# Optimization experiments

Measured on AMD Instinct MI355X. Metric: run time of the kernel, lower is better.

Reference implementation:

```python
import jax, jax.numpy as jnp
import numpy as np

B = 1024          # batch of subject-object pairs
D_IN_HALF = 2048  # sbj/obj feature width; cat -> input_len = 4096
D_OUT = 1024      # output_len (embedding / label-vec width)
N_LABELS = 128    # number of relation labels in codebook


def setup_inputs() -> dict:
    key = jax.random.key(0)
    ks = jax.random.split(key, 7)
    s = 0.02  # small init scale for weights
    return {
        "sbj_vec": jax.random.normal(ks[0], (B, D_IN_HALF), jnp.float32),
        "obj_vec": jax.random.normal(ks[1], (B, D_IN_HALF), jnp.float32),
        "W1": jax.random.normal(ks[2], (2 * D_IN_HALF, D_OUT), jnp.float32) * s,
        "b1": jax.random.normal(ks[3], (D_OUT,), jnp.float32) * s,
        "W2": jax.random.normal(ks[4], (D_OUT, D_OUT), jnp.float32) * s,
        "b2": jax.random.normal(ks[5], (D_OUT,), jnp.float32) * s,
        "label_vecs": jax.random.normal(ks[6], (N_LABELS, D_OUT), jnp.float32),
    }


def reference(sbj_vec, obj_vec, W1, b1, W2, b2, label_vecs):
    # Sequential(ReLU, Dropout(eval=identity), Linear) applied twice.
    x = jnp.concatenate([sbj_vec, obj_vec], axis=1)          # [B, 2*D_IN_HALF]
    hidden = jax.nn.relu(x) @ W1 + b1                        # [B, D_OUT]
    emb = jax.nn.relu(hidden) @ W2 + b2                      # [B, D_OUT]
    # order_sim vs every label vector, fully batched (replaces per-sample loop):
    # sim[b, l] = -|| relu(label_vecs[l] - emb[b]) ||_2
    diff = jax.nn.relu(label_vecs[None, :, :] - emb[:, None, :])  # [B, L, D_OUT]
    scores = -jnp.sqrt(jnp.sum(diff * diff, axis=2))              # [B, L]
    return scores
```

## Files before the change

### kernel.cpp

```cpp
#include <hip/hip_runtime.h>
#include <math.h>

constexpr int Bn = 1024, DH = 2048, K1 = 4096, DO = 1024, NL = 128;
constexpr int MN = Bn * DO;

typedef __bf16 bf16x8 __attribute__((ext_vector_type(8)));
typedef short  s16x8  __attribute__((ext_vector_type(8)));
typedef float  f32x4  __attribute__((ext_vector_type(4)));

__device__ __forceinline__ unsigned short f2bf(float f) {
  union { float f; unsigned u; } v; v.f = f;
  unsigned r = v.u + 0x7FFFu + ((v.u >> 16) & 1u);
  return (unsigned short)(r >> 16);
}

__global__ __launch_bounds__(256)
void prep(const float* __restrict__ sbj, const float* __restrict__ obj,
          const float* __restrict__ W1, const float* __restrict__ W2,
          unsigned short* __restrict__ Abf,
          unsigned short* __restrict__ W1t, unsigned short* __restrict__ W2t) {
  const int tid = threadIdx.x;
  if (blockIdx.x < 2048) {
    const int t = blockIdx.x * 256 + tid;
    const int m = t >> 9;
    const int k = (t & 511) << 3;
    const float* src = (k < DH) ? sbj + (size_t)m * DH + k
                                : obj + (size_t)m * DH + (k - DH);
    const float4 a = ((const float4*)src)[0];
    const float4 b = ((const float4*)src)[1];
    uint4 o;
    o.x = (unsigned)f2bf(fmaxf(a.x, 0.f)) | ((unsigned)f2bf(fmaxf(a.y, 0.f)) << 16);
    o.y = (unsigned)f2bf(fmaxf(a.z, 0.f)) | ((unsigned)f2bf(fmaxf(a.w, 0.f)) << 16);
    o.z = (unsigned)f2bf(fmaxf(b.x, 0.f)) | ((unsigned)f2bf(fmaxf(b.y, 0.f)) << 16);
    o.w = (unsigned)f2bf(fmaxf(b.z, 0.f)) | ((unsigned)f2bf(fmaxf(b.w, 0.f)) << 16);
    *(uint4*)&Abf[(size_t)m * K1 + k] = o;
    return;
  }
  __shared__ float tl[64][65];
  const int tb = blockIdx.x - 2048;
  int by = tb >> 4;
  const int c0 = (tb & 15) * 64;
  const float* in; unsigned short* out; int R;
  if (by < 64) { in = W1; out = W1t; R = K1; }
  else         { in = W2; out = W2t; R = DO; by -= 64; }
  const int r0 = by * 64;
  {
    const int rr = tid >> 4, cc = (tid & 15) * 4;
    #pragma unroll
    for (int i = 0; i < 4; ++i) {
      const float4 v = *(const float4*)&in[(size_t)(r0 + rr + i * 16) * DO + c0 + cc];
      tl[rr + i * 16][cc + 0] = v.x; tl[rr + i * 16][cc + 1] = v.y;
      tl[rr + i * 16][cc + 2] = v.z; tl[rr + i * 16][cc + 3] = v.w;
    }
  }
  __syncthreads();
  {
    const int r4 = (tid & 15) * 4;
    #pragma unroll
    for (int i = 0; i < 4; ++i) {
      const int cr = i * 16 + (tid >> 4);
      uint2 o;
      o.x = (unsigned)f2bf(tl[r4 + 0][cr]) | ((unsigned)f2bf(tl[r4 + 1][cr]) << 16);
      o.y = (unsigned)f2bf(tl[r4 + 2][cr]) | ((unsigned)f2bf(tl[r4 + 3][cr]) << 16);
      *(uint2*)&out[(size_t)(c0 + cr) * R + r0 + r4] = o;
    }
  }
}

template <int KSLICE>
__global__ __launch_bounds__(256, 4)
void mfma_gemm(const unsigned short* __restrict__ A,
               const unsigned short* __restrict__ Bt,
               float* __restrict__ P, int K) {
  __shared__ __align__(16) unsigned short smem[2 * 64 * 128];
  unsigned short* LA = smem;
  unsigned short* LB = smem + 64 * 128;

  const int tid = threadIdx.x;
  const int w = tid >> 6, l = tid & 63;

  const int bid = blockIdx.x;
  const int g = bid & 7, t = bid >> 3;
  const int x = (g & 3) * 4 + (t & 3);
  const int y = (g >> 2) * 8 + ((t >> 2) & 7);
  const int z = t >> 5;
  const int m0 = y * 64, n0 = x * 64;
  const int kb = z * KSLICE;

  f32x4 acc[4][4] = {};

  constexpr int NIT = KSLICE / 128;
  for (int it = 0; it < NIT; ++it) {
    const int k0 = kb + it * 128;
    #pragma unroll
    for (int i = 0; i < 4; ++i) {
      const int c = i * 256 + tid, m = c >> 4, kc = c & 15;
      const int kcg = (kc & 8) | ((kc & 7) ^ (m & 7));
      __builtin_amdgcn_global_load_lds(
          (const __attribute__((address_space(1))) unsigned int*)(A + (size_t)(m0 + m) * K + k0 + kcg * 8),
          (__attribute__((address_space(3))) unsigned int*)&LA[c * 8], 16, 0, 0);
    }
    #pragma unroll
    for (int i = 0; i < 4; ++i) {
      const int c = i * 256 + tid, n = c >> 4, kc = c & 15;
      const int kcg = (kc & 8) | ((kc & 7) ^ (n & 7));
      __builtin_amdgcn_global_load_lds(
          (const __attribute__((address_space(1))) unsigned int*)(Bt + (size_t)(n0 + n) * K + k0 + kcg * 8),
          (__attribute__((address_space(3))) unsigned int*)&LB[c * 8], 16, 0, 0);
    }
    __syncthreads();

    const int kcq = w * 4 + (l >> 4);
    bf16x8 af[4], bfr[4];
    #pragma unroll
    for (int i = 0; i < 4; ++i) {
      const int r = i * 16 + (l & 15);
      const int kca = (kcq & 8) | ((kcq & 7) ^ (r & 7));
      af[i]  = __builtin_bit_cast(bf16x8, *(const s16x8*)&LA[(r * 16 + kca) * 8]);
      bfr[i] = __builtin_bit_cast(bf16x8, *(const s16x8*)&LB[(r * 16 + kca) * 8]);
    }
    #pragma unroll
    for (int i = 0; i < 4; ++i)
      #pragma unroll
      for (int j = 0; j < 4; ++j)
        acc[i][j] = __builtin_amdgcn_mfma_f32_16x16x32_bf16(af[i], bfr[j], acc[i][j], 0, 0, 0);
    __syncthreads();
  }

  float* red = (float*)smem;
  if (w >= 2) {
    #pragma unroll
    for (int i = 0; i < 4; ++i)
      #pragma unroll
      for (int j = 0; j < 4; ++j)
        *(f32x4*)&red[(w - 2) * 4096 + ((i * 4 + j) * 64 + l) * 4] = acc[i][j];
  }
  __syncthreads();
  if (w < 2) {
    #pragma unroll
    for (int i = 0; i < 4; ++i)
      #pragma unroll
      for (int j = 0; j < 4; ++j)
        acc[i][j] += *(const f32x4*)&red[w * 4096 + ((i * 4 + j) * 64 + l) * 4];
  }
  __syncthreads();
  if (w == 1) {
    #pragma unroll
    for (int i = 0; i < 2; ++i)
      #pragma unroll
      for (int j = 0; j < 4; ++j)
        *(f32x4*)&red[((i * 4 + j) * 64 + l) * 4] = acc[i][j];
  } else if (w == 0) {
    #pragma unroll
    for (int i = 0; i < 2; ++i)
      #pragma unroll
      for (int j = 0; j < 4; ++j)
        *(f32x4*)&red[2048 + ((i * 4 + j) * 64 + l) * 4] = acc[i + 2][j];
  }
  __syncthreads();
  if (w >= 2) return;

  float* Pz = P + (size_t)z * MN;
  if (w == 0) {
    #pragma unroll
    for (int i = 0; i < 2; ++i) {
      #pragma unroll
      for (int j = 0; j < 4; ++j)
        acc[i][j] += *(const f32x4*)&red[((i * 4 + j) * 64 + l) * 4];
      #pragma unroll
      for (int r = 0; r < 4; ++r) {
        const int m = m0 + i * 16 + (l >> 4) * 4 + r;
        #pragma unroll
        for (int j = 0; j < 4; ++j)
          Pz[(size_t)m * DO + n0 + j * 16 + (l & 15)] = acc[i][j][r];
      }
    }
  } else {
    #pragma unroll
    for (int i = 0; i < 2; ++i) {
      #pragma unroll
      for (int j = 0; j < 4; ++j)
        acc[i + 2][j] += *(const f32x4*)&red[2048 + ((i * 4 + j) * 64 + l) * 4];
      #pragma unroll
      for (int r = 0; r < 4; ++r) {
        const int m = m0 + (i + 2) * 16 + (l >> 4) * 4 + r;
        #pragma unroll
        for (int j = 0; j < 4; ++j)
          Pz[(size_t)m * DO + n0 + j * 16 + (l & 15)] = acc[i + 2][j][r];
      }
    }
  }
}

template <int KS, bool RELU, bool OUT_BF16>
__global__ __launch_bounds__(256)
void combine(const float* __restrict__ P, const float* __restrict__ bias,
             void* __restrict__ out) {
  const int row = blockIdx.x, t = threadIdx.x;
  const size_t i4 = (size_t)row * 256 + t;
  f32x4 s = ((const f32x4*)P)[i4];
  #pragma unroll
  for (int c = 1; c < KS; ++c) s += ((const f32x4*)P)[(size_t)c * (MN / 4) + i4];
  const f32x4 bb = *(const f32x4*)&bias[t * 4];
  s += bb;
  if (RELU) {
    s[0] = fmaxf(s[0], 0.f); s[1] = fmaxf(s[1], 0.f);
    s[2] = fmaxf(s[2], 0.f); s[3] = fmaxf(s[3], 0.f);
  }
  if (OUT_BF16) {
    uint2 o;
    o.x = (unsigned)f2bf(s[0]) | ((unsigned)f2bf(s[1]) << 16);
    o.y = (unsigned)f2bf(s[2]) | ((unsigned)f2bf(s[3]) << 16);
    *(uint2*)((unsigned short*)out + (size_t)row * DO + t * 4) = o;
  } else {
    *(f32x4*)((float*)out + (size_t)row * DO + t * 4) = s;
  }
}

__global__ __launch_bounds__(256)
void score_partial(const float* __restrict__ P, const float* __restrict__ b2,
                   const float* __restrict__ labels, float* __restrict__ SP) {
  __shared__ float es[64][33];
  __shared__ float ls[64][132];
  const int tid = threadIdx.x;
  const int b0 = blockIdx.x * 32;
  const int d0 = blockIdx.y * 64;

  #pragma unroll
  for (int i = 0; i < 2; ++i) {
    const int fi = tid + i * 256;
    const int b = fi >> 4, dq = fi & 15;
    const size_t idx = ((size_t)(b0 + b) * DO + d0 + dq * 4) / 4;
    f32x4 v = ((const f32x4*)P)[idx];
    #pragma unroll
    for (int c = 1; c < 4; ++c) v += ((const f32x4*)P)[(size_t)c * (MN / 4) + idx];
    v += *(const f32x4*)&b2[d0 + dq * 4];
    es[dq * 4 + 0][b] = v[0]; es[dq * 4 + 1][b] = v[1];
    es[dq * 4 + 2][b] = v[2]; es[dq * 4 + 3][b] = v[3];
  }
  #pragma unroll
  for (int i = 0; i < 8; ++i) {
    const int fi = tid + i * 256;
    const int lr = fi >> 4, dq = fi & 15;
    const float4 v = *(const float4*)&labels[(size_t)lr * DO + d0 + dq * 4];
    ls[dq * 4 + 0][lr] = v.x; ls[dq * 4 + 1][lr] = v.y;
    ls[dq * 4 + 2][lr] = v.z; ls[dq * 4 + 3][lr] = v.w;
  }
  __syncthreads();

  const int tb = tid & 15;
  const int tl = tid >> 4;
  float acc[2][8] = {};

  for (int dd = 0; dd < 64; ++dd) {
    const float e0 = es[dd][tb * 2 + 0];
    const float e1 = es[dd][tb * 2 + 1];
    const float4 l0 = *(const float4*)&ls[dd][tl * 8];
    const float4 l1 = *(const float4*)&ls[dd][tl * 8 + 4];
    const float lv[8] = {l0.x, l0.y, l0.z, l0.w, l1.x, l1.y, l1.z, l1.w};
    #pragma unroll
    for (int j = 0; j < 8; ++j) {
      float t0 = fmaxf(lv[j] - e0, 0.f); acc[0][j] = fmaf(t0, t0, acc[0][j]);
      float t1 = fmaxf(lv[j] - e1, 0.f); acc[1][j] = fmaf(t1, t1, acc[1][j]);
    }
  }

  float* SPz = SP + (size_t)blockIdx.y * (Bn * NL);
  #pragma unroll
  for (int i = 0; i < 2; ++i) {
    const size_t base = (size_t)(b0 + tb * 2 + i) * NL + tl * 8;
    float4 v0 = {acc[i][0], acc[i][1], acc[i][2], acc[i][3]};
    float4 v1 = {acc[i][4], acc[i][5], acc[i][6], acc[i][7]};
    *(float4*)&SPz[base]     = v0;
    *(float4*)&SPz[base + 4] = v1;
  }
}

__global__ __launch_bounds__(256)
void score_reduce(const float* __restrict__ SP, float* __restrict__ out) {
  const size_t i4 = (size_t)blockIdx.x * 256 + threadIdx.x;
  f32x4 s = ((const f32x4*)SP)[i4];
  #pragma unroll
  for (int c = 1; c < 16; ++c) s += ((const f32x4*)SP)[(size_t)c * 32768 + i4];
  f32x4 o = {-sqrtf(s[0]), -sqrtf(s[1]), -sqrtf(s[2]), -sqrtf(s[3])};
  ((f32x4*)out)[i4] = o;
}

extern "C" void kernel_launch(void* const* d_in, const int* in_sizes, int n_in,
                              void* d_out, int out_size, void* d_ws, size_t ws_size,
                              hipStream_t stream) {
  const float* sbj  = (const float*)d_in[0];
  const float* obj  = (const float*)d_in[1];
  const float* W1   = (const float*)d_in[2];
  const float* b1   = (const float*)d_in[3];
  const float* W2   = (const float*)d_in[4];
  const float* b2   = (const float*)d_in[5];
  const float* labs = (const float*)d_in[6];
  float* scores = (float*)d_out;

  char* ws = (char*)d_ws;
  unsigned short* Abf = (unsigned short*)(ws);
  unsigned short* W1t = (unsigned short*)(ws + (8ull << 20));
  unsigned short* W2t = (unsigned short*)(ws + (16ull << 20));
  unsigned short* H   = (unsigned short*)(ws + (18ull << 20));
  float* P  = (float*)(ws + (24ull << 20));
  float* SP = (float*)(ws + (40ull << 20));

  dim3 blk(256);
  prep<<<dim3(2048 + 1280), blk, 0, stream>>>(sbj, obj, W1, W2, Abf, W1t, W2t);

  mfma_gemm<1024><<<dim3(1024), blk, 0, stream>>>(Abf, W1t, P, K1);
  combine<4, true, true><<<dim3(Bn), blk, 0, stream>>>(P, b1, H);
  mfma_gemm<256><<<dim3(1024), blk, 0, stream>>>(H, W2t, P, DO);
  score_partial<<<dim3(32, 16), blk, 0, stream>>>(P, b2, labs, SP);
  score_reduce<<<dim3(128), blk, 0, stream>>>(SP, scores);
}
```

Before: 141.0 us.

## Retile GEMM1 to 128x128 tiles with 8-way split-K; run GEMM2 without split-K

GEMM1 now uses 128x128 output tiles with a 64-wide K step and 8 K-slices. Each wave computes its own 64x64 quadrant, so the in-block LDS reduction is gone and each loaded element is reused more. GEMM2 runs with full K in 256 blocks and adds the bias in its epilogue, writing the embedding directly, so score_partial no longer sums four partial buffers. In exchange, GEMM1 writes and combine1 reads 8 fp32 partial buffers instead of 4. GEMM2 has less parallelism, and GEMM1 occupancy drops to 2 blocks per SIMD-set.

```diff
diff --git a/kernel.cpp b/kernel.cpp
--- a/kernel.cpp
+++ b/kernel.cpp
@@ -68,36 +68,124 @@
 }
 
 template <int KSLICE>
-__global__ __launch_bounds__(256, 4)
+__global__ __launch_bounds__(256, 2)
 void mfma_gemm(const unsigned short* __restrict__ A,
                const unsigned short* __restrict__ Bt,
                float* __restrict__ P, int K) {
+  __shared__ __align__(16) unsigned short smem[2 * 128 * 64];
+  unsigned short* LA = smem;
+  unsigned short* LB = smem + 128 * 64;
+
+  const int tid = threadIdx.x;
+  const int w = tid >> 6, l = tid & 63;
+  const int bid = blockIdx.x;
+  const int z = bid & 7, t = bid >> 3;
+  const int m0 = (t >> 3) * 128, n0 = (t & 7) * 128;
+  const int kb = z * KSLICE;
+
+  f32x4 acc[4][4] = {};
+
+  constexpr int NIT = KSLICE / 64;
+  for (int it = 0; it < NIT; ++it) {
+    const int k0 = kb + it * 64;
+    #pragma unroll
+    for (int i = 0; i < 4; ++i) {
+      const int c = i * 256 + tid, row = c >> 3, kc = c & 7;
+      const int kcg = kc ^ (row & 7);
+      __builtin_amdgcn_global_load_lds(
+          (const __attribute__((address_space(1))) unsigned int*)(A + (size_t)(m0 + row) * K + k0 + kcg * 8),
+          (__attribute__((address_space(3))) unsigned int*)&LA[c * 8], 16, 0, 0);
+    }
+    #pragma unroll
+    for (int i = 0; i < 4; ++i) {
+      const int c = i * 256 + tid, row = c >> 3, kc = c & 7;
+      const int kcg = kc ^ (row & 7);
+      __builtin_amdgcn_global_load_lds(
+          (const __attribute__((address_space(1))) unsigned int*)(Bt + (size_t)(n0 + row) * K + k0 + kcg * 8),
+          (__attribute__((address_space(3))) unsigned int*)&LB[c * 8], 16, 0, 0);
+    }
+    __syncthreads();
+
+    #pragma unroll
+    for (int s = 0; s < 2; ++s) {
+      const int kcq = s * 4 + (l >> 4);
+      bf16x8 af[4], bfr[4];
+      #pragma unroll
+      for (int i = 0; i < 4; ++i) {
+        const int r = (w >> 1) * 64 + i * 16 + (l & 15);
+        const int kca = kcq ^ (r & 7);
+        af[i] = __builtin_bit_cast(bf16x8, *(const s16x8*)&LA[(r * 8 + kca) * 8]);
+      }
+      #pragma unroll
+      for (int j = 0; j < 4; ++j) {
+        const int rr = (w & 1) * 64 + j * 16 + (l & 15);
+        const int kcb = kcq ^ (rr & 7);
+        bfr[j] = __builtin_bit_cast(bf16x8, *(const s16x8*)&LB[(rr * 8 + kcb) * 8]);
+      }
+      #pragma unroll
+      for (int i = 0; i < 4; ++i)
+        #pragma unroll
+        for (int j = 0; j < 4; ++j)
+          acc[i][j] = __builtin_amdgcn_mfma_f32_16x16x32_bf16(af[i], bfr[j], acc[i][j], 0, 0, 0);
+    }
+    __syncthreads();
+  }
+
+  float* Pz = P + (size_t)z * MN;
+  #pragma unroll
+  for (int i = 0; i < 4; ++i) {
+    #pragma unroll
+    for (int r = 0; r < 4; ++r) {
+      const int m = m0 + (w >> 1) * 64 + i * 16 + (l >> 4) * 4 + r;
+      #pragma unroll
+      for (int j = 0; j < 4; ++j) {
+        const int n = n0 + (w & 1) * 64 + j * 16 + (l & 15);
+        Pz[(size_t)m * DO + n] = acc[i][j][r];
+      }
+    }
+  }
+}
+
+__global__ __launch_bounds__(256)
+void combine1(const float* __restrict__ P, const float* __restrict__ bias,
+              unsigned short* __restrict__ out) {
+  const int row = blockIdx.x, t = threadIdx.x;
+  const size_t i4 = (size_t)row * 256 + t;
+  f32x4 s = ((const f32x4*)P)[i4];
+  #pragma unroll
+  for (int c = 1; c < 8; ++c) s += ((const f32x4*)P)[(size_t)c * (MN / 4) + i4];
+  s += *(const f32x4*)&bias[t * 4];
+  s[0] = fmaxf(s[0], 0.f); s[1] = fmaxf(s[1], 0.f);
+  s[2] = fmaxf(s[2], 0.f); s[3] = fmaxf(s[3], 0.f);
+  uint2 o;
+  o.x = (unsigned)f2bf(s[0]) | ((unsigned)f2bf(s[1]) << 16);
+  o.y = (unsigned)f2bf(s[2]) | ((unsigned)f2bf(s[3]) << 16);
+  *(uint2*)&out[(size_t)row * DO + t * 4] = o;
+}
+
+__global__ __launch_bounds__(256, 4)
+void gemm2_full(const unsigned short* __restrict__ A,
+                const unsigned short* __restrict__ Bt,
+                const float* __restrict__ b2, float* __restrict__ E) {
   __shared__ __align__(16) unsigned short smem[2 * 64 * 128];
   unsigned short* LA = smem;
   unsigned short* LB = smem + 64 * 128;
 
   const int tid = threadIdx.x;
   const int w = tid >> 6, l = tid & 63;
-
   const int bid = blockIdx.x;
-  const int g = bid & 7, t = bid >> 3;
-  const int x = (g & 3) * 4 + (t & 3);
-  const int y = (g >> 2) * 8 + ((t >> 2) & 7);
-  const int z = t >> 5;
-  const int m0 = y * 64, n0 = x * 64;
-  const int kb = z * KSLICE;
+  const int m0 = (bid >> 4) * 64, n0 = (bid & 15) * 64;
 
   f32x4 acc[4][4] = {};
 
-  constexpr int NIT = KSLICE / 128;
-  for (int it = 0; it < NIT; ++it) {
-    const int k0 = kb + it * 128;
+  for (int it = 0; it < 8; ++it) {
+    const int k0 = it * 128;
     #pragma unroll
     for (int i = 0; i < 4; ++i) {
       const int c = i * 256 + tid, m = c >> 4, kc = c & 15;
       const int kcg = (kc & 8) | ((kc & 7) ^ (m & 7));
       __builtin_amdgcn_global_load_lds(
-          (const __attribute__((address_space(1))) unsigned int*)(A + (size_t)(m0 + m) * K + k0 + kcg * 8),
+          (const __attribute__((address_space(1))) unsigned int*)(A + (size_t)(m0 + m) * DO + k0 + kcg * 8),
           (__attribute__((address_space(3))) unsigned int*)&LA[c * 8], 16, 0, 0);
     }
     #pragma unroll
@@ -105,7 +193,7 @@
       const int c = i * 256 + tid, n = c >> 4, kc = c & 15;
       const int kcg = (kc & 8) | ((kc & 7) ^ (n & 7));
       __builtin_amdgcn_global_load_lds(
-          (const __attribute__((address_space(1))) unsigned int*)(Bt + (size_t)(n0 + n) * K + k0 + kcg * 8),
+          (const __attribute__((address_space(1))) unsigned int*)(Bt + (size_t)(n0 + n) * DO + k0 + kcg * 8),
           (__attribute__((address_space(3))) unsigned int*)&LB[c * 8], 16, 0, 0);
     }
     __syncthreads();
@@ -160,7 +248,6 @@
   __syncthreads();
   if (w >= 2) return;
 
-  float* Pz = P + (size_t)z * MN;
   if (w == 0) {
     #pragma unroll
     for (int i = 0; i < 2; ++i) {
@@ -171,8 +258,10 @@
       for (int r = 0; r < 4; ++r) {
         const int m = m0 + i * 16 + (l >> 4) * 4 + r;
         #pragma unroll
-        for (int j = 0; j < 4; ++j)
-          Pz[(size_t)m * DO + n0 + j * 16 + (l & 15)] = acc[i][j][r];
+        for (int j = 0; j < 4; ++j) {
+          const int n = n0 + j * 16 + (l & 15);
+          E[(size_t)m * DO + n] = acc[i][j][r] + b2[n];
+        }
       }
     }
   } else {
@@ -185,41 +274,18 @@
       for (int r = 0; r < 4; ++r) {
         const int m = m0 + (i + 2) * 16 + (l >> 4) * 4 + r;
         #pragma unroll
-        for (int j = 0; j < 4; ++j)
-          Pz[(size_t)m * DO + n0 + j * 16 + (l & 15)] = acc[i + 2][j][r];
-      }
-    }
-  }
-}
-
-template <int KS, bool RELU, bool OUT_BF16>
+        for (int j = 0; j < 4; ++j) {
+          const int n = n0 + j * 16 + (l & 15);
+          E[(size_t)m * DO + n] = acc[i + 2][j][r] + b2[n];
+        }
+      }
+    }
+  }
+}
+
 __global__ __launch_bounds__(256)
-void combine(const float* __restrict__ P, const float* __restrict__ bias,
-             void* __restrict__ out) {
-  const int row = blockIdx.x, t = threadIdx.x;
-  const size_t i4 = (size_t)row * 256 + t;
-  f32x4 s = ((const f32x4*)P)[i4];
-  #pragma unroll
-  for (int c = 1; c < KS; ++c) s += ((const f32x4*)P)[(size_t)c * (MN / 4) + i4];
-  const f32x4 bb = *(const f32x4*)&bias[t * 4];
-  s += bb;
-  if (RELU) {
-    s[0] = fmaxf(s[0], 0.f); s[1] = fmaxf(s[1], 0.f);
-    s[2] = fmaxf(s[2], 0.f); s[3] = fmaxf(s[3], 0.f);
-  }
-  if (OUT_BF16) {
-    uint2 o;
-    o.x = (unsigned)f2bf(s[0]) | ((unsigned)f2bf(s[1]) << 16);
-    o.y = (unsigned)f2bf(s[2]) | ((unsigned)f2bf(s[3]) << 16);
-    *(uint2*)((unsigned short*)out + (size_t)row * DO + t * 4) = o;
-  } else {
-    *(f32x4*)((float*)out + (size_t)row * DO + t * 4) = s;
-  }
-}
-
-__global__ __launch_bounds__(256)
-void score_partial(const float* __restrict__ P, const float* __restrict__ b2,
-                   const float* __restrict__ labels, float* __restrict__ SP) {
+void score_partial(const float* __restrict__ E, const float* __restrict__ labels,
+                   float* __restrict__ SP) {
   __shared__ float es[64][33];
   __shared__ float ls[64][132];
   const int tid = threadIdx.x;
@@ -230,13 +296,9 @@
   for (int i = 0; i < 2; ++i) {
     const int fi = tid + i * 256;
     const int b = fi >> 4, dq = fi & 15;
-    const size_t idx = ((size_t)(b0 + b) * DO + d0 + dq * 4) / 4;
-    f32x4 v = ((const f32x4*)P)[idx];
-    #pragma unroll
-    for (int c = 1; c < 4; ++c) v += ((const f32x4*)P)[(size_t)c * (MN / 4) + idx];
-    v += *(const f32x4*)&b2[d0 + dq * 4];
-    es[dq * 4 + 0][b] = v[0]; es[dq * 4 + 1][b] = v[1];
-    es[dq * 4 + 2][b] = v[2]; es[dq * 4 + 3][b] = v[3];
+    const float4 v = *(const float4*)&E[(size_t)(b0 + b) * DO + d0 + dq * 4];
+    es[dq * 4 + 0][b] = v.x; es[dq * 4 + 1][b] = v.y;
+    es[dq * 4 + 2][b] = v.z; es[dq * 4 + 3][b] = v.w;
   }
   #pragma unroll
   for (int i = 0; i < 8; ++i) {
@@ -297,21 +359,22 @@
   const float* b2   = (const float*)d_in[5];
   const float* labs = (const float*)d_in[6];
   float* scores = (float*)d_out;
-
   char* ws = (char*)d_ws;
+
   unsigned short* Abf = (unsigned short*)(ws);
   unsigned short* W1t = (unsigned short*)(ws + (8ull << 20));
   unsigned short* W2t = (unsigned short*)(ws + (16ull << 20));
   unsigned short* H   = (unsigned short*)(ws + (18ull << 20));
+  float* E  = (float*)(ws + (20ull << 20));
   float* P  = (float*)(ws + (24ull << 20));
-  float* SP = (float*)(ws + (40ull << 20));
+  float* SP = (float*)(ws + (56ull << 20));
 
   dim3 blk(256);
   prep<<<dim3(2048 + 1280), blk, 0, stream>>>(sbj, obj, W1, W2, Abf, W1t, W2t);
 
-  mfma_gemm<1024><<<dim3(1024), blk, 0, stream>>>(Abf, W1t, P, K1);
-  combine<4, true, true><<<dim3(Bn), blk, 0, stream>>>(P, b1, H);
-  mfma_gemm<256><<<dim3(1024), blk, 0, stream>>>(H, W2t, P, DO);
-  score_partial<<<dim3(32, 16), blk, 0, stream>>>(P, b2, labs, SP);
+  mfma_gemm<512><<<dim3(512), blk, 0, stream>>>(Abf, W1t, P, K1);
+  combine1<<<dim3(Bn), blk, 0, stream>>>(P, b1, H);
+  gemm2_full<<<dim3(256), blk, 0, stream>>>(H, W2t, b2, E);
+  score_partial<<<dim3(32, 16), blk, 0, stream>>>(E, labs, SP);
   score_reduce<<<dim3(128), blk, 0, stream>>>(SP, scores);
 }
```

Measured after the change: 136.5 us. -3.2%, faster.
